# Kernel tuning notes

Measured on AMD Instinct MI355X. Metric: run time of the kernel, lower is better.

## Reference

```python
import jax, jax.numpy as jnp
import numpy as np

DIM = 1024
INTER = 2048
N_EXPERTS = 8
TOP_K = 2
ROUTE_SCALE = 1.0


def setup_inputs() -> dict:
    key = jax.random.key(0)
    ks = jax.random.split(key, 4)
    x = jax.random.normal(ks[0], (4, 2048, DIM), dtype=jnp.float32)
    # Gate weight matches nn.Parameter(torch.randn(n_experts, dim))
    Wg = jax.random.normal(ks[1], (N_EXPERTS, DIM), dtype=jnp.float32)
    W1 = jax.random.normal(ks[2], (N_EXPERTS, DIM, INTER), dtype=jnp.float32) * (1.0 / np.sqrt(DIM))
    b1 = jnp.zeros((N_EXPERTS, INTER), dtype=jnp.float32)
    W2 = jax.random.normal(ks[3], (N_EXPERTS, INTER, DIM), dtype=jnp.float32) * (1.0 / np.sqrt(INTER))
    b2 = jnp.zeros((N_EXPERTS, DIM), dtype=jnp.float32)
    return {"x": x, "Wg": Wg, "W1": W1, "b1": b1, "W2": W2, "b2": b2}


def reference(x, Wg, W1, b1, W2, b2):
    # Flatten tokens: [T, D]
    xt = x.reshape(-1, DIM)
    T = xt.shape[0]

    # --- Gate: sigmoid scores, top-k, normalized weights ---
    scores = jax.nn.sigmoid(xt @ Wg.T)                       # [T, E]
    top_w, top_idx = jax.lax.top_k(scores, TOP_K)            # [T, K]
    top_w = top_w / jnp.sum(top_w, axis=-1, keepdims=True)
    top_w = top_w * ROUTE_SCALE

    # Sparse combine weights [T, E] (top_k indices are distinct per token)
    cw = jnp.zeros((T, N_EXPERTS), dtype=xt.dtype)
    cw = cw.at[jnp.arange(T)[:, None], top_idx].set(top_w)

    # --- Experts: dense per-expert MLP, weighted combine ---
    # (dropout is identity in eval mode)
    h = jax.nn.relu(jnp.einsum('td,edh->eth', xt, W1) + b1[:, None, :])   # [E, T, H]
    eo = jnp.einsum('eth,ehd->etd', h, W2) + b2[:, None, :]               # [E, T, D]
    y = jnp.einsum('etd,te->td', eo, cw)                                  # [T, D]
    return y
```

## Files before the change

kernel.cpp:

```cpp
#include <hip/hip_runtime.h>
#include <stdint.h>

#define DIM   1024
#define INTER 2048
#define NEXP  8

typedef _Float16 f16;
typedef __attribute__((ext_vector_type(4))) _Float16 f16x4;
typedef __attribute__((ext_vector_type(8))) _Float16 f16x8;
typedef __attribute__((ext_vector_type(4))) float    f32x4;

static __device__ __forceinline__ void gload16(const void* gsrc, void* lds) {
    __builtin_amdgcn_global_load_lds(
        (const __attribute__((address_space(1))) uint32_t*)gsrc,
        (__attribute__((address_space(3))) uint32_t*)lds,
        16, 0, 0);
}

__global__ void gate_convert_kernel(const float* __restrict__ x, const float* __restrict__ Wg,
                                    f16* __restrict__ xh, float* __restrict__ gw,
                                    int* __restrict__ gidx, int T) {
    const int tok  = (int)((blockIdx.x * (size_t)blockDim.x + threadIdx.x) >> 6);
    const int lane = threadIdx.x & 63;
    if (tok >= T) return;
    const float4* xr  = (const float4*)(x + (size_t)tok * DIM);
    f16*          xhr = xh + (size_t)tok * DIM;
    float s[NEXP];
    #pragma unroll
    for (int e = 0; e < NEXP; ++e) s[e] = 0.f;
    #pragma unroll
    for (int it = 0; it < 4; ++it) {
        int i = it * 64 + lane;
        float4 xv = xr[i];
        f16x4 hv = { (f16)xv.x, (f16)xv.y, (f16)xv.z, (f16)xv.w };
        *(f16x4*)(xhr + i * 4) = hv;
        #pragma unroll
        for (int e = 0; e < NEXP; ++e) {
            float4 wv = ((const float4*)(Wg + e * DIM))[i];
            s[e] += xv.x * wv.x + xv.y * wv.y + xv.z * wv.z + xv.w * wv.w;
        }
    }
    #pragma unroll
    for (int e = 0; e < NEXP; ++e) {
        #pragma unroll
        for (int off = 32; off > 0; off >>= 1) s[e] += __shfl_xor(s[e], off);
    }
    if (lane == 0) {
        float sc[NEXP];
        #pragma unroll
        for (int e = 0; e < NEXP; ++e) sc[e] = 1.f / (1.f + expf(-s[e]));
        int i0 = 0;
        #pragma unroll
        for (int e = 1; e < NEXP; ++e) if (sc[e] > sc[i0]) i0 = e;
        int i1 = -1;
        #pragma unroll
        for (int e = 0; e < NEXP; ++e) if (e != i0 && (i1 < 0 || sc[e] > sc[i1])) i1 = e;
        float w0 = sc[i0], w1 = sc[i1];
        float inv = 1.f / (w0 + w1);
        gw[2 * tok + 0] = w0 * inv;
        gw[2 * tok + 1] = w1 * inv;
        gidx[2 * tok + 0] = i0;
        gidx[2 * tok + 1] = i1;
    }
}

__global__ void transpose_conv_kernel(const float* __restrict__ W, f16* __restrict__ Wt, int K, int N) {
    __shared__ f16 tile[64][65];
    const int e  = blockIdx.z;
    const int kb = blockIdx.y * 64;
    const int nb = blockIdx.x * 64;
    const int tx = threadIdx.x & 63;
    const int ty = threadIdx.x >> 6;
    const float* We  = W  + (size_t)e * K * N;
    f16*         Wte = Wt + (size_t)e * K * N;
    #pragma unroll
    for (int i = 0; i < 16; ++i) {
        int k = ty + i * 4;
        tile[k][tx] = (f16)We[(size_t)(kb + k) * N + nb + tx];
    }
    __syncthreads();
    #pragma unroll
    for (int i = 0; i < 16; ++i) {
        int n = ty + i * 4;
        Wte[(size_t)(nb + n) * K + kb + tx] = tile[tx][n];
    }
}

__global__ __launch_bounds__(1024)
void route_kernel(const int* __restrict__ gidx, int* __restrict__ offsets,
                  int* __restrict__ tor, int* __restrict__ ros, int T) {
    const int tid  = threadIdx.x;
    const int lane = tid & 63;
    const int wv   = tid >> 6;
    const int NE   = 2 * T;
    __shared__ int wc[16][NEXP];
    __shared__ int rb[NEXP];

    int c[NEXP];
    #pragma unroll
    for (int e = 0; e < NEXP; ++e) c[e] = 0;
    for (int i = tid; i < NE; i += 1024) {
        int g = gidx[i];
        #pragma unroll
        for (int e = 0; e < NEXP; ++e) c[e] += (g == e) ? 1 : 0;
    }
    #pragma unroll
    for (int e = 0; e < NEXP; ++e) {
        #pragma unroll
        for (int off = 32; off > 0; off >>= 1) c[e] += __shfl_xor(c[e], off);
    }
    if (lane == 0) {
        #pragma unroll
        for (int e = 0; e < NEXP; ++e) wc[wv][e] = c[e];
    }
    __syncthreads();
    if (tid == 0) {
        int acc = 0;
        for (int e = 0; e < NEXP; ++e) {
            int t = 0;
            for (int w2 = 0; w2 < 16; ++w2) t += wc[w2][e];
            offsets[e] = acc;
            rb[e] = acc;
            acc += t;
        }
        offsets[NEXP] = acc;
    }
    __syncthreads();

    for (int base = 0; base < NE; base += 1024) {
        int i = base + tid;
        int g = gidx[i];
        int myrank = 0;
        #pragma unroll
        for (int e = 0; e < NEXP; ++e) {
            unsigned long long m = __ballot(g == e);
            if (g == e) myrank = __popcll(m & ((1ull << lane) - 1ull));
            if (lane == 0) wc[wv][e] = __popcll(m);
        }
        __syncthreads();
        int pre = 0;
        for (int w2 = 0; w2 < wv; ++w2) pre += wc[w2][g];
        int pos = rb[g] + pre + myrank;
        tor[pos] = i >> 1;
        ros[i]   = pos;
        __syncthreads();
        if (tid < NEXP) {
            int t = 0;
            for (int w2 = 0; w2 < 16; ++w2) t += wc[w2][tid];
            rb[tid] += t;
        }
        __syncthreads();
    }
}

template<int KD, int ND, bool RELU, bool GATHER, int RT>
__global__ __launch_bounds__(256)
void moe_gemm_kernel(const f16* __restrict__ Abase, const f16* __restrict__ Bt,
                     const float* __restrict__ bias, const int* __restrict__ offsets,
                     const int* __restrict__ tok, f16* __restrict__ Cout) {
    constexpr int NT = ND / 128;
    const int cpx = (NT * RT * NEXP) >> 3;
    const int bid = blockIdx.x;
    const int lg  = (bid & 7) * cpx + (bid >> 3);
    const int nt  = lg % NT;
    const int tmp = lg / NT;
    const int rt  = tmp % RT;
    const int e   = tmp / RT;

    const int rowBeg = offsets[e];
    const int rowEnd = offsets[e + 1];
    const int row0   = rowBeg + rt * 128;
    if (row0 >= rowEnd) return;
    const int n0   = nt * 128;
    const int tid  = threadIdx.x;
    const int lane = tid & 63;
    const int wid  = tid >> 6;
    const int wr   = (wid >> 1) * 64;
    const int wc   = (wid & 1) * 64;

    __shared__ __align__(16) f16 As[128 * 32];
    __shared__ __align__(16) f16 Bs[128 * 32];

    const f16* Bte = Bt + (size_t)e * ND * KD;

    int arow[2];
    #pragma unroll
    for (int i = 0; i < 2; ++i) {
        int c  = i * 256 + tid;
        int r  = c >> 2;
        int gr = row0 + r;
        if (gr >= rowEnd) gr = rowEnd - 1;
        arow[i] = GATHER ? tok[gr] : gr;
    }

    f32x4 acc[4][4] = {};

    const int nK = KD / 32;
    for (int kt = 0; kt < nK; ++kt) {
        const int k0 = kt * 32;
        #pragma unroll
        for (int i = 0; i < 2; ++i) {
            int c  = i * 256 + tid;
            int kc = (c & 3) ^ ((c >> 3) & 3);
            gload16(Abase + (size_t)arow[i] * KD + k0 + kc * 8, &As[c * 8]);
        }
        #pragma unroll
        for (int i = 0; i < 2; ++i) {
            int c = i * 256 + tid;
            int r = c >> 2, kc = (c & 3) ^ ((c >> 3) & 3);
            gload16(Bte + (size_t)(n0 + r) * KD + k0 + kc * 8, &Bs[c * 8]);
        }
        __syncthreads();

        const int sl   = ((lane >> 4) ^ ((lane >> 1) & 3)) * 8;
        f16x8 af[4], bfr[4];
        #pragma unroll
        for (int m = 0; m < 4; ++m)
            af[m] = *(const f16x8*)&As[(wr + m * 16 + (lane & 15)) * 32 + sl];
        #pragma unroll
        for (int n = 0; n < 4; ++n)
            bfr[n] = *(const f16x8*)&Bs[(wc + n * 16 + (lane & 15)) * 32 + sl];
        #pragma unroll
        for (int m = 0; m < 4; ++m)
            #pragma unroll
            for (int n = 0; n < 4; ++n)
                acc[m][n] = __builtin_amdgcn_mfma_f32_16x16x32_f16(af[m], bfr[n], acc[m][n], 0, 0, 0);
        __syncthreads();
    }

    const int rowsValid = rowEnd - row0;
    #pragma unroll
    for (int m = 0; m < 4; ++m) {
        #pragma unroll
        for (int n = 0; n < 4; ++n) {
            #pragma unroll
            for (int j = 0; j < 4; ++j) {
                int rl  = wr + m * 16 + ((lane >> 4) << 2) + j;
                int col = n0 + wc + n * 16 + (lane & 15);
                if (rl < rowsValid) {
                    float v = acc[m][n][j] + bias[e * ND + col];
                    if (RELU) v = fmaxf(v, 0.f);
                    Cout[(size_t)(row0 + rl) * ND + col] = (f16)v;
                }
            }
        }
    }
}

__global__ void combine_kernel(const f16* __restrict__ eo, const int* __restrict__ ros,
                               const float* __restrict__ gw, float* __restrict__ y, int T) {
    int gid = blockIdx.x * 256 + threadIdx.x;
    int t   = gid >> 7;
    if (t >= T) return;
    int c0 = (gid & 127) * 8;
    int r0 = ros[2 * t], r1 = ros[2 * t + 1];
    float w0 = gw[2 * t], w1 = gw[2 * t + 1];
    f16x8 v0 = *(const f16x8*)(eo + (size_t)r0 * DIM + c0);
    f16x8 v1 = *(const f16x8*)(eo + (size_t)r1 * DIM + c0);
    f32x4 o0, o1;
    #pragma unroll
    for (int j = 0; j < 4; ++j) o0[j] = w0 * (float)v0[j] + w1 * (float)v1[j];
    #pragma unroll
    for (int j = 0; j < 4; ++j) o1[j] = w0 * (float)v0[4 + j] + w1 * (float)v1[4 + j];
    *(f32x4*)(y + (size_t)t * DIM + c0)     = o0;
    *(f32x4*)(y + (size_t)t * DIM + c0 + 4) = o1;
}

extern "C" void kernel_launch(void* const* d_in, const int* in_sizes, int n_in,
                              void* d_out, int out_size, void* d_ws, size_t ws_size,
                              hipStream_t stream) {
    const float* x  = (const float*)d_in[0];
    const float* Wg = (const float*)d_in[1];
    const float* W1 = (const float*)d_in[2];
    const float* b1 = (const float*)d_in[3];
    const float* W2 = (const float*)d_in[4];
    const float* b2 = (const float*)d_in[5];
    float* y = (float*)d_out;
    const int T = in_sizes[0] / DIM;

    char* ws = (char*)d_ws;
    size_t off = 0;
    auto alloc = [&](size_t bytes) -> char* {
        char* p = ws + off;
        off += (bytes + 255) & ~(size_t)255;
        return p;
    };
    f16* xh   = (f16*)alloc((size_t)T * DIM * 2);
    f16* w1t  = (f16*)alloc((size_t)NEXP * DIM * INTER * 2);
    f16* w2t  = (f16*)alloc((size_t)NEXP * DIM * INTER * 2);
    f16* h    = (f16*)alloc((size_t)2 * T * INTER * 2);
    f16* eo   = (f16*)alloc((size_t)2 * T * DIM * 2);
    float* gw = (float*)alloc((size_t)T * 2 * 4);
    int* gidx = (int*)alloc((size_t)T * 2 * 4);
    int* ros  = (int*)alloc((size_t)T * 2 * 4);
    int* tor  = (int*)alloc((size_t)2 * T * 4);
    int* offsets = (int*)alloc(64 * 4);

    gate_convert_kernel<<<T / 4, 256, 0, stream>>>(x, Wg, xh, gw, gidx, T);
    transpose_conv_kernel<<<dim3(INTER / 64, DIM / 64, NEXP), 256, 0, stream>>>(W1, w1t, DIM, INTER);
    transpose_conv_kernel<<<dim3(DIM / 64, INTER / 64, NEXP), 256, 0, stream>>>(W2, w2t, INTER, DIM);
    route_kernel<<<1, 1024, 0, stream>>>(gidx, offsets, tor, ros, T);
    moe_gemm_kernel<DIM, INTER, true, true, 64>
        <<<dim3((INTER / 128) * 64 * NEXP), 256, 0, stream>>>(xh, w1t, b1, offsets, tor, h);
    moe_gemm_kernel<INTER, DIM, false, false, 64>
        <<<dim3((DIM / 128) * 64 * NEXP), 256, 0, stream>>>(h, w2t, b2, offsets, tor, eo);
    combine_kernel<<<(T * DIM / 8 + 255) / 256, 256, 0, stream>>>(eo, ros, gw, y, T);
}
```

Before: 371.8 us.

## Triple-buffer LDS tiles with async prefetch and remap blocks across XCDs

The MoE GEMM main loop becomes a 3-stage LDS ring. Global-to-LDS loads for tile k+2 are issued before computing tile k, and a vmcnt wait plus a single barrier per iteration replaces the two syncthreads. This is meant to hide global load latency behind MFMA work. The block-to-tile mapping also changes so that each XCD gets a 4x2 patch of row and column tiles within an expert, aiming for better L2 reuse. LDS use triples, which may lower occupancy, and the remap assumes RT is divisible by 4 and NT by 2.

```diff
diff --git a/kernel.cpp b/kernel.cpp
--- a/kernel.cpp
+++ b/kernel.cpp
@@ -158,14 +158,19 @@
 void moe_gemm_kernel(const f16* __restrict__ Abase, const f16* __restrict__ Bt,
                      const float* __restrict__ bias, const int* __restrict__ offsets,
                      const int* __restrict__ tok, f16* __restrict__ Cout) {
-    constexpr int NT = ND / 128;
-    const int cpx = (NT * RT * NEXP) >> 3;
+    constexpr int NT  = ND / 128;
+    constexpr int NT2 = NT / 2;
+    constexpr int RT4 = RT / 4;
     const int bid = blockIdx.x;
-    const int lg  = (bid & 7) * cpx + (bid >> 3);
-    const int nt  = lg % NT;
-    const int tmp = lg / NT;
-    const int rt  = tmp % RT;
-    const int e   = tmp / RT;
+    const int xcd = bid & 7;
+    const int rtl = xcd >> 1;
+    const int ntl = xcd & 1;
+    const int j   = bid >> 3;
+    const int nth = j % NT2;
+    const int rth = (j / NT2) % RT4;
+    const int e   = j / (NT2 * RT4);
+    const int nt  = nth * 2 + ntl;
+    const int rt  = rth * 4 + rtl;
 
     const int rowBeg = offsets[e];
     const int rowEnd = offsets[e + 1];
@@ -178,55 +183,68 @@
     const int wr   = (wid >> 1) * 64;
     const int wc   = (wid & 1) * 64;
 
-    __shared__ __align__(16) f16 As[128 * 32];
-    __shared__ __align__(16) f16 Bs[128 * 32];
+    __shared__ __align__(16) f16 As[3][128 * 32];
+    __shared__ __align__(16) f16 Bs[3][128 * 32];
 
     const f16* Bte = Bt + (size_t)e * ND * KD;
 
-    int arow[2];
+    const f16* Aptr[2];
+    const f16* Bptr[2];
     #pragma unroll
     for (int i = 0; i < 2; ++i) {
         int c  = i * 256 + tid;
         int r  = c >> 2;
+        int kc = (c & 3) ^ ((c >> 3) & 3);
         int gr = row0 + r;
         if (gr >= rowEnd) gr = rowEnd - 1;
-        arow[i] = GATHER ? tok[gr] : gr;
-    }
-
+        int ar = GATHER ? tok[gr] : gr;
+        Aptr[i] = Abase + (size_t)ar * KD + kc * 8;
+        Bptr[i] = Bte + (size_t)(n0 + r) * KD + kc * 8;
+    }
+
+    auto stage = [&](int buf, int kt) {
+        const int k0 = kt * 32;
+        #pragma unroll
+        for (int i = 0; i < 2; ++i)
+            gload16(Aptr[i] + k0, &As[buf][(i * 256 + tid) * 8]);
+        #pragma unroll
+        for (int i = 0; i < 2; ++i)
+            gload16(Bptr[i] + k0, &Bs[buf][(i * 256 + tid) * 8]);
+    };
+
+    constexpr int nK = KD / 32;
     f32x4 acc[4][4] = {};
 
-    const int nK = KD / 32;
+    stage(0, 0);
+    stage(1, nK > 1 ? 1 : 0);
+
+    const int sl = ((lane >> 4) ^ ((lane >> 1) & 3)) * 8;
+
+    int cb = 0, sbuf = 2, ktn = (2 < nK) ? 2 : nK - 1;
     for (int kt = 0; kt < nK; ++kt) {
-        const int k0 = kt * 32;
-        #pragma unroll
-        for (int i = 0; i < 2; ++i) {
-            int c  = i * 256 + tid;
-            int kc = (c & 3) ^ ((c >> 3) & 3);
-            gload16(Abase + (size_t)arow[i] * KD + k0 + kc * 8, &As[c * 8]);
-        }
-        #pragma unroll
-        for (int i = 0; i < 2; ++i) {
-            int c = i * 256 + tid;
-            int r = c >> 2, kc = (c & 3) ^ ((c >> 3) & 3);
-            gload16(Bte + (size_t)(n0 + r) * KD + k0 + kc * 8, &Bs[c * 8]);
-        }
-        __syncthreads();
-
-        const int sl   = ((lane >> 4) ^ ((lane >> 1) & 3)) * 8;
+        asm volatile("s_waitcnt vmcnt(4)" ::: "memory");
+        __builtin_amdgcn_s_barrier();
+        stage(sbuf, ktn);
+        ktn  = (ktn + 1 < nK) ? ktn + 1 : nK - 1;
+        sbuf = (sbuf == 2) ? 0 : sbuf + 1;
+
+        const f16* Asb = As[cb];
+        const f16* Bsb = Bs[cb];
         f16x8 af[4], bfr[4];
         #pragma unroll
         for (int m = 0; m < 4; ++m)
-            af[m] = *(const f16x8*)&As[(wr + m * 16 + (lane & 15)) * 32 + sl];
+            af[m] = *(const f16x8*)&Asb[(wr + m * 16 + (lane & 15)) * 32 + sl];
         #pragma unroll
         for (int n = 0; n < 4; ++n)
-            bfr[n] = *(const f16x8*)&Bs[(wc + n * 16 + (lane & 15)) * 32 + sl];
+            bfr[n] = *(const f16x8*)&Bsb[(wc + n * 16 + (lane & 15)) * 32 + sl];
         #pragma unroll
         for (int m = 0; m < 4; ++m)
             #pragma unroll
             for (int n = 0; n < 4; ++n)
                 acc[m][n] = __builtin_amdgcn_mfma_f32_16x16x32_f16(af[m], bfr[n], acc[m][n], 0, 0, 0);
-        __syncthreads();
-    }
+        cb = (cb == 2) ? 0 : cb + 1;
+    }
+    asm volatile("s_waitcnt vmcnt(0)" ::: "memory");
 
     const int rowsValid = rowEnd - row0;
     #pragma unroll
@@ -234,11 +252,11 @@
         #pragma unroll
         for (int n = 0; n < 4; ++n) {
             #pragma unroll
-            for (int j = 0; j < 4; ++j) {
-                int rl  = wr + m * 16 + ((lane >> 4) << 2) + j;
+            for (int j2 = 0; j2 < 4; ++j2) {
+                int rl  = wr + m * 16 + ((lane >> 4) << 2) + j2;
                 int col = n0 + wc + n * 16 + (lane & 15);
                 if (rl < rowsValid) {
-                    float v = acc[m][n][j] + bias[e * ND + col];
+                    float v = acc[m][n][j2] + bias[e * ND + col];
                     if (RELU) v = fmaxf(v, 0.f);
                     Cout[(size_t)(row0 + rl) * ND + col] = (f16)v;
                 }
```

After: 363.9 us. 1.02x faster.
